# Performance work log

Measured on AMD Instinct MI355X. Metric: run time of the kernel, lower is better.

Reference implementation:

```python
import jax, jax.numpy as jnp
import numpy as np

N_NODES = 10000
N_EDGES = 160000
MUL = 128          # channel multiplicity
N_SPECIES = 10
SH_OFF = [0, 1, 4, 9, 16]   # spherical-harmonic offsets for l=0..3 (2l+1 each)
RADIAL_IN = 8
SIN_DIM = 32
MAX_DENSITY = 100.0


def setup_inputs() -> dict:
    key = jax.random.key(0)
    ks = jax.random.split(key, 16)
    inp = {
        'node_attrs': jax.random.normal(ks[0], (N_NODES, N_SPECIES), jnp.float32),
        'node_feats': jax.random.normal(ks[1], (N_NODES, MUL), jnp.float32),
        'edge_attrs': jax.random.normal(ks[2], (N_EDGES, 16), jnp.float32),
        'edge_feats': jax.random.normal(ks[3], (N_EDGES, RADIAL_IN), jnp.float32),
        'edge_index': jax.random.randint(ks[4], (2, N_EDGES), 0, N_NODES, jnp.int64),
        'W_up': jax.random.normal(ks[5], (MUL, MUL), jnp.float32),
        'Wr1': jax.random.normal(ks[6], (RADIAL_IN, 64), jnp.float32),
        'Wr2': jax.random.normal(ks[7], (64, 64), jnp.float32),
        'Wr3': jax.random.normal(ks[8], (64, 64), jnp.float32),
        'Wr4': jax.random.normal(ks[9], (64, 4 * MUL), jnp.float32),
        'Wd': jax.random.normal(ks[10], (RADIAL_IN, 1), jnp.float32),
        'Wsin': jax.random.normal(ks[11], (SIN_DIM, MUL), jnp.float32),
        'Wlin': jax.random.normal(ks[12], (4, MUL, MUL), jnp.float32),
        'Wskip': jax.random.normal(ks[13], (4, MUL, N_SPECIES, MUL), jnp.float32),
    }
    return inp


def _sinusoidal_embedding(x):
    # continuous sinusoidal embedding: dim=32, max_density=100
    half = SIN_DIM // 2
    freqs = jnp.exp(-jnp.log(MAX_DENSITY) * jnp.arange(half, dtype=x.dtype) / half)
    ang = x[:, None] * freqs[None, :]          # [N, 16]
    return jnp.concatenate([jnp.sin(ang), jnp.cos(ang)], axis=-1)  # [N, 32]


def reference(node_attrs, node_feats, edge_attrs, edge_feats, edge_index,
              W_up, Wr1, Wr2, Wr3, Wr4, Wd, Wsin, Wlin, Wskip):
    N = node_feats.shape[0]
    sender, receiver = edge_index[0], edge_index[1]

    # linear_up (e3nn o3.Linear on 128x0e, fan-in normalized)
    x = node_feats @ (W_up / np.float32(np.sqrt(MUL)))          # [N, 128]

    # radial MLP: FullyConnectedNet([8,64,64,64,512], silu), fan-in normalized
    h = edge_feats
    for W in (Wr1, Wr2, Wr3):
        h = jax.nn.silu(h @ (W / np.float32(np.sqrt(W.shape[0]))))
    tp_w = (h @ (Wr4 / np.float32(np.sqrt(64)))).reshape(-1, 4, MUL)  # [E, 4, 128]

    # equivariant TP: scalar node feats (x) gathered by sender, uvu path per SH l
    xs = x[sender]                                              # [E, 128]
    weighted = xs[:, None, :] * tp_w                            # [E, 4, 128]
    blocks = []
    for l in range(4):
        sh_l = edge_attrs[:, SH_OFF[l]:SH_OFF[l + 1]]           # [E, 2l+1]
        blk = weighted[:, l, :, None] * sh_l[:, None, :]        # [E, 128, 2l+1]
        blocks.append(blk.reshape(blk.shape[0], -1))
    mji = jnp.concatenate(blocks, axis=-1)                      # [E, 2048]

    # per-edge density gate
    density = jnp.tanh((edge_feats @ Wd) ** 2)                  # [E, 1]

    # scatter-sum messages and density to receivers
    message = jax.ops.segment_sum(mji, receiver, num_segments=N)        # [N, 2048]
    rho = jax.ops.segment_sum(density, receiver, num_segments=N)       # [N, 1]
    message = message / (rho + 1.0)

    # density embedding injected into the l=0 block
    demb = _sinusoidal_embedding(rho[:, 0]) @ Wsin              # [N, 128]
    message = message.at[:, :MUL].add(demb)

    # per-l linear (irreps_mid -> irreps_out), skip_tp with node_attrs, reshape
    out_blocks = []
    for l in range(4):
        d = 2 * l + 1
        blk = message[:, MUL * SH_OFF[l]:MUL * SH_OFF[l + 1]].reshape(N, MUL, d)
        blk = jnp.einsum('nuk,uv->nvk', blk, Wlin[l]) / np.float32(np.sqrt(MUL))
        blk = jnp.einsum('nvk,na,vaw->nwk', blk, node_attrs, Wskip[l]) \
              / np.float32(np.sqrt(MUL * N_SPECIES))
        out_blocks.append(blk)
    return jnp.concatenate(out_blocks, axis=-1)                 # [N, 128, 16]
```

## Files before the change

### kernel.cpp

```cpp
#include <hip/hip_runtime.h>
#include <hip/hip_bf16.h>

#define N_NODES 10000
#define N_EDGES 160000

typedef _Float16 h8 __attribute__((ext_vector_type(8)));
typedef _Float16 h4 __attribute__((ext_vector_type(4)));
typedef float f32x4 __attribute__((ext_vector_type(4)));

__device__ __forceinline__ float silu_f(float v){ return v / (1.f + expf(-v)); }

__global__ __launch_bounds__(256) void k_pre(const float* __restrict__ Wr2,
                                             const float* __restrict__ Wr3,
                                             const float* __restrict__ Wr4,
                                             const float* __restrict__ Wup,
                                             const float* __restrict__ Wlin,
                                             const float* __restrict__ Wskip,
                                             const int* __restrict__ eidx,
                                             _Float16* __restrict__ Wr2T,
                                             _Float16* __restrict__ Wr3T,
                                             _Float16* __restrict__ Wr4T,
                                             _Float16* __restrict__ WupT,
                                             _Float16* __restrict__ WC16T,
                                             int* __restrict__ cnt){
  const int b = blockIdx.x;
  __shared__ float wl[128];
  if (b < 224){
    const int idx = b*256 + threadIdx.x;
    if (idx < 4096){
      const int n = idx >> 6, k = idx & 63;
      Wr2T[idx] = (_Float16)(Wr2[k*64 + n] * 0.125f);
    } else if (idx < 8192){
      const int j = idx - 4096;
      const int n = j >> 6, k = j & 63;
      Wr3T[j] = (_Float16)(Wr3[k*64 + n] * 0.125f);
    } else if (idx < 40960){
      const int j = idx - 8192;
      const int n = j >> 6, k = j & 63;
      Wr4T[j] = (_Float16)(Wr4[k*512 + n] * 0.125f);
    } else if (idx < 57344){
      const int j = idx - 40960;
      const int u = j >> 7, k = j & 127;
      WupT[j] = (_Float16)(Wup[k*128 + u] * 0.08838834764831843f);
    }
  } else if (b < 736){
    const int lu = b - 224;
    const int l  = lu >> 7, u = lu & 127;
    if (threadIdx.x < 128) wl[threadIdx.x] = Wlin[lu*128 + threadIdx.x];
    __syncthreads();
    const float* Wsk = Wskip + (size_t)l * 163840;
    for (int i = threadIdx.x; i < 1280; i += 256){
      float acc = 0.f;
      #pragma unroll 16
      for (int v = 0; v < 128; ++v) acc += wl[v] * Wsk[v*1280 + i];
      const int a = i >> 7, w = i & 127;
      WC16T[((size_t)l*128 + w)*1280 + a*128 + u] =
          (_Float16)(acc * 0.0024705294220065465f);
    }
  } else {
    const int e = (b - 736)*256 + threadIdx.x;
    if (e < N_EDGES) atomicAdd(&cnt[eidx[N_EDGES + e]], 1);
  }
}

__global__ __launch_bounds__(256) void k_scan(const int* __restrict__ cnt,
                                              int* __restrict__ off,
                                              int* __restrict__ cur){
  __shared__ int sums[256];
  const int t = threadIdx.x;
  const int base = t * 40;
  int s = 0;
  for (int i = 0; i < 40; ++i){
    const int idx = base + i;
    if (idx < N_NODES) s += cnt[idx];
  }
  sums[t] = s;
  __syncthreads();
  for (int st = 1; st < 256; st <<= 1){
    const int v = (t >= st) ? sums[t - st] : 0;
    __syncthreads();
    sums[t] += v;
    __syncthreads();
  }
  int pre = (t > 0) ? sums[t - 1] : 0;
  for (int i = 0; i < 40; ++i){
    const int idx = base + i;
    if (idx < N_NODES){
      off[idx] = pre; cur[idx] = pre;
      pre += cnt[idx];
    }
  }
  if (t == 255) off[N_NODES] = sums[255];
}

__global__ __launch_bounds__(256) void k_mid(const int* __restrict__ eidx,
                                             const float* __restrict__ ef,
                                             const float* __restrict__ ea,
                                             int* __restrict__ cur,
                                             int* __restrict__ esnd,
                                             float* __restrict__ efp,
                                             float* __restrict__ eap,
                                             const float* __restrict__ nf,
                                             const _Float16* __restrict__ WupT,
                                             float* __restrict__ x){
  const int b = blockIdx.x;
  const int tid = threadIdx.x;
  alignas(16) __shared__ _Float16 s_nf[64*128];
  alignas(16) __shared__ _Float16 s_wt[128*128];

  if (b < 625){
    const int e = b * 256 + tid;
    if (e < N_EDGES){
      const int pos = atomicAdd(&cur[eidx[N_EDGES + e]], 1);
      esnd[pos] = eidx[e];
      const float4* efs = (const float4*)(ef + (size_t)e*8);
      float4* efd = (float4*)(efp + (size_t)pos*8);
      efd[0] = efs[0]; efd[1] = efs[1];
      const float4* eas = (const float4*)(ea + (size_t)e*16);
      float4* ead = (float4*)(eap + (size_t)pos*16);
      ead[0] = eas[0]; ead[1] = eas[1]; ead[2] = eas[2]; ead[3] = eas[3];
    }
    return;
  }

  const int n0 = (b - 625) * 64;
  {
    const int rl = tid >> 2, part = tid & 3;
    const int gr = n0 + rl;
    #pragma unroll
    for (int j = 0; j < 4; ++j){
      const int cu = part*4 + j;
      h8 hv = (h8){};
      if (gr < N_NODES){
        const float4 v0 = *(const float4*)(nf + (size_t)gr*128 + cu*8);
        const float4 v1 = *(const float4*)(nf + (size_t)gr*128 + cu*8 + 4);
        hv[0]=(_Float16)v0.x; hv[1]=(_Float16)v0.y; hv[2]=(_Float16)v0.z; hv[3]=(_Float16)v0.w;
        hv[4]=(_Float16)v1.x; hv[5]=(_Float16)v1.y; hv[6]=(_Float16)v1.z; hv[7]=(_Float16)v1.w;
      }
      const int cs = (cu & 8) | ((cu & 7) ^ (rl & 7));
      *(h8*)&s_nf[rl*128 + cs*8] = hv;
    }
  }
  {
    const int rl = tid >> 1, part = tid & 1;
    #pragma unroll
    for (int j = 0; j < 8; ++j){
      const int cu = part*8 + j;
      const h8 v = *(const h8*)&WupT[(size_t)rl*128 + cu*8];
      const int cs = (cu & 8) | ((cu & 7) ^ (rl & 7));
      *(h8*)&s_wt[rl*128 + cs*8] = v;
    }
  }
  __syncthreads();

  const int wid = tid >> 6, lane = tid & 63;
  const int li = lane & 15, kg = lane >> 4;

  f32x4 acc[8];
  #pragma unroll
  for (int i = 0; i < 8; ++i) acc[i] = (f32x4){0,0,0,0};

  const int row = wid*16 + li;
  #pragma unroll
  for (int s = 0; s < 4; ++s){
    const int ca = s*4 + kg;
    const int csA = (ca & 8) | ((ca & 7) ^ (row & 7));
    const h8 af = *(const h8*)&s_nf[row*128 + csA*8];
    #pragma unroll
    for (int nt = 0; nt < 8; ++nt){
      const int u = nt*16 + li;
      const int csB = (ca & 8) | ((ca & 7) ^ (u & 7));
      const h8 bf = *(const h8*)&s_wt[u*128 + csB*8];
      acc[nt] = __builtin_amdgcn_mfma_f32_16x16x32_f16(af, bf, acc[nt], 0, 0, 0);
    }
  }
  #pragma unroll
  for (int nt = 0; nt < 8; ++nt){
    #pragma unroll
    for (int r = 0; r < 4; ++r){
      const int gr = n0 + wid*16 + kg*4 + r;
      if (gr < N_NODES) x[(size_t)gr*128 + nt*16 + li] = acc[nt][r];
    }
  }
}

__global__ __launch_bounds__(256) void k_fused(const float* __restrict__ efp,
                                               const float* __restrict__ eap,
                                               const float* __restrict__ x,
                                               const float* __restrict__ Wr1,
                                               const float* __restrict__ Wd,
                                               const _Float16* __restrict__ Wr2T,
                                               const _Float16* __restrict__ Wr3T,
                                               const _Float16* __restrict__ Wr4T,
                                               const float* __restrict__ Wsin,
                                               const int* __restrict__ off,
                                               const int* __restrict__ esnd,
                                               _Float16* __restrict__ msg16){
  const int n0 = blockIdx.x * 4;
  const int tid = threadIdx.x;
  const int lane = tid & 63, wid = tid >> 6;
  const int li = lane & 15, kg = lane >> 4;
  const int u = tid & 127, h = tid >> 7;

  __shared__ float s_ef[32][8];
  __shared__ float s_w1[8][64];
  alignas(16) __shared__ _Float16 s_xs[32][132];
  alignas(16) __shared__ _Float16 s_actA[32][64];
  alignas(16) __shared__ _Float16 s_actB[32][64];
  alignas(16) __shared__ _Float16 s_w2[32][264];
  alignas(16) __shared__ float s_sh[2][32][16];
  __shared__ float s_dd[32];
  __shared__ float s_rho[4];
  __shared__ int   s_offs[5];
  __shared__ float s_emb[4][32];

  if (tid < 5) s_offs[tid] = off[n0 + tid];
  if (tid < 4) s_rho[tid] = 0.f;
  for (int j = tid; j < 512; j += 256) s_w1[j >> 6][j & 63] = Wr1[j];
  __syncthreads();

  const int beg = s_offs[0], end = s_offs[4];
  const int ngrp = (end - beg + 31) >> 5;

  const int e8 = tid >> 3, i8 = tid & 7;
  const int slotB = tid >> 4, jjB = tid & 15;

  float a0[8] = {0,0,0,0,0,0,0,0};
  float a1[8] = {0,0,0,0,0,0,0,0};
  float a2[8] = {0,0,0,0,0,0,0,0};
  float a3[8] = {0,0,0,0,0,0,0,0};

  if (ngrp > 0){
    const int p = beg + e8;
    s_ef[e8][i8] = (p < end) ? efp[(size_t)p*8 + i8] : 0.f;
    const int pB0 = beg + slotB, pB1 = beg + slotB + 16;
    s_sh[0][slotB][jjB]      = (pB0 < end) ? eap[(size_t)pB0*16 + jjB] : 0.f;
    s_sh[0][slotB + 16][jjB] = (pB1 < end) ? eap[(size_t)pB1*16 + jjB] : 0.f;
    const int snd = (p < end) ? esnd[p] : 0;
    const float4* xp = (const float4*)(x + (size_t)snd*128 + i8*16);
    #pragma unroll
    for (int j = 0; j < 4; ++j){
      const float4 v = xp[j];
      h4 hv; hv[0]=(_Float16)v.x; hv[1]=(_Float16)v.y; hv[2]=(_Float16)v.z; hv[3]=(_Float16)v.w;
      *(h4*)&s_xs[e8][i8*16 + j*4] = hv;
    }
  }
  __syncthreads();

  for (int g = 0; g < ngrp; ++g){
    const int cur = g & 1, nxt = cur ^ 1;
    const int pbase  = beg + g*32;
    const int pbase2 = pbase + 32;
    const bool more = (g + 1 < ngrp);

    float ef_r = 0.f, sh_r0 = 0.f, sh_r1 = 0.f;
    int snd_r = 0;
    const int pA = pbase2 + e8;
    const bool vA = more && (pA < end);
    if (vA){ ef_r = efp[(size_t)pA*8 + i8]; snd_r = esnd[pA]; }
    const int pB0 = pbase2 + slotB, pB1 = pbase2 + slotB + 16;
    if (more && pB0 < end) sh_r0 = eap[(size_t)pB0*16 + jjB];
    if (more && pB1 < end) sh_r1 = eap[(size_t)pB1*16 + jjB];

    if (tid < 32){
      float s = 0.f;
      #pragma unroll
      for (int i = 0; i < 8; ++i) s += s_ef[tid][i] * Wd[i];
      s_dd[tid] = tanhf(s*s);
    }

    {
      const int e = tid >> 3, ng = tid & 7;
      float hv[8] = {0,0,0,0,0,0,0,0};
      #pragma unroll
      for (int k = 0; k < 8; ++k){
        const float ev = s_ef[e][k] * 0.3535533905932738f;
        #pragma unroll
        for (int j = 0; j < 8; ++j) hv[j] += ev * s_w1[k][ng*8 + j];
      }
      h8 o;
      #pragma unroll
      for (int j = 0; j < 8; ++j) o[j] = (_Float16)silu_f(hv[j]);
      *(h8*)&s_actA[e][(ng ^ (e & 7))*8] = o;
    }
    __syncthreads();

    if (more) s_ef[e8][i8] = ef_r;

    {
      h8 af[2];
      #pragma unroll
      for (int s = 0; s < 2; ++s)
        af[s] = *(const h8*)&Wr2T[(size_t)(wid*16 + li)*64 + s*32 + kg*8];
      #pragma unroll
      for (int nt = 0; nt < 2; ++nt){
        const int e = nt*16 + li;
        f32x4 acc = (f32x4){0,0,0,0};
        #pragma unroll
        for (int s = 0; s < 2; ++s){
          const h8 bf = *(const h8*)&s_actA[e][((s*4 + kg) ^ (e & 7))*8];
          acc = __builtin_amdgcn_mfma_f32_16x16x32_f16(af[s], bf, acc, 0, 0, 0);
        }
        #pragma unroll
        for (int r = 0; r < 4; ++r){
          const int n = wid*16 + kg*4 + r;
          s_actB[e][((n >> 3) ^ (e & 7))*8 + (n & 7)] = (_Float16)silu_f(acc[r]);
        }
      }
    }
    __syncthreads();

    float4 xs_r0 = {0,0,0,0}, xs_r1 = {0,0,0,0}, xs_r2 = {0,0,0,0}, xs_r3 = {0,0,0,0};
    if (vA){
      const float4* xp = (const float4*)(x + (size_t)snd_r*128 + i8*16);
      xs_r0 = xp[0]; xs_r1 = xp[1]; xs_r2 = xp[2]; xs_r3 = xp[3];
    }

    {
      h8 af[2];
      #pragma unroll
      for (int s = 0; s < 2; ++s)
        af[s] = *(const h8*)&Wr3T[(size_t)(wid*16 + li)*64 + s*32 + kg*8];
      #pragma unroll
      for (int nt = 0; nt < 2; ++nt){
        const int e = nt*16 + li;
        f32x4 acc = (f32x4){0,0,0,0};
        #pragma unroll
        for (int s = 0; s < 2; ++s){
          const h8 bf = *(const h8*)&s_actB[e][((s*4 + kg) ^ (e & 7))*8];
          acc = __builtin_amdgcn_mfma_f32_16x16x32_f16(af[s], bf, acc, 0, 0, 0);
        }
        #pragma unroll
        for (int r = 0; r < 4; ++r){
          const int n = wid*16 + kg*4 + r;
          s_actA[e][((n >> 3) ^ (e & 7))*8 + (n & 7)] = (_Float16)silu_f(acc[r]);
        }
      }
    }
    __syncthreads();

    int lo0 = s_offs[0] - pbase; lo0 = lo0 < 0 ? 0 : lo0;
    int hi0 = s_offs[1] - pbase; hi0 = hi0 > 32 ? 32 : (hi0 < 0 ? 0 : hi0);
    int lo1 = s_offs[1] - pbase; lo1 = lo1 < 0 ? 0 : lo1;
    int hi1 = s_offs[2] - pbase; hi1 = hi1 > 32 ? 32 : (hi1 < 0 ? 0 : hi1);
    int lo2 = s_offs[2] - pbase; lo2 = lo2 < 0 ? 0 : lo2;
    int hi2 = s_offs[3] - pbase; hi2 = hi2 > 32 ? 32 : (hi2 < 0 ? 0 : hi2);
    int lo3 = s_offs[3] - pbase; lo3 = lo3 < 0 ? 0 : lo3;
    int hi3 = s_offs[4] - pbase; hi3 = hi3 > 32 ? 32 : (hi3 < 0 ? 0 : hi3);

    h8 bf[2][2];
    #pragma unroll
    for (int nt = 0; nt < 2; ++nt){
      const int e = nt*16 + li;
      #pragma unroll
      for (int s = 0; s < 2; ++s)
        bf[nt][s] = *(const h8*)&s_actA[e][((s*4 + kg) ^ (e & 7))*8];
    }

#define ACCA(A, LO, HI)                                              \
    for (int s = (LO); s < (HI); ++s){                               \
      const float wa  = (float)s_w2[s][u];                           \
      const float wb  = (float)s_w2[s][128 + u];                     \
      const float4 sa = *(const float4*)&s_sh[cur][s][0];            \
      A[0] += wa*sa.x;                                               \
      A[1] += wb*sa.y;  A[2] += wb*sa.z;  A[3] += wb*sa.w;           \
    }
#define ACCB0(A, LO, HI)                                             \
    for (int s = (LO); s < (HI); ++s){                               \
      const float wcv = (float)s_w2[s][u];                           \
      const float4 sb = *(const float4*)&s_sh[cur][s][4];            \
      A[4] += wcv*sb.x; A[5] += wcv*sb.y;                            \
      A[6] += wcv*sb.z; A[7] += wcv*sb.w;                            \
    }
#define ACCB1(A, LO, HI)                                             \
    for (int s = (LO); s < (HI); ++s){                               \
      const float wcv = (float)s_w2[s][u];                           \
      const float wd  = (float)s_w2[s][128 + u];                     \
      const float4 sa = *(const float4*)&s_sh[cur][s][8];            \
      const float4 sb = *(const float4*)&s_sh[cur][s][12];           \
      A[0] += wcv*sa.x;                                              \
      A[1] += wd*sa.y;  A[2] += wd*sa.z;  A[3] += wd*sa.w;           \
      A[4] += wd*sb.x;  A[5] += wd*sb.y;                             \
      A[6] += wd*sb.z;  A[7] += wd*sb.w;                             \
    }

    #pragma unroll
    for (int pass = 0; pass < 2; ++pass){
      #pragma unroll
      for (int mt = 0; mt < 4; ++mt){
        const int cc0 = wid*64 + mt*16;
        const int nb  = pass*256 + cc0;
        h8 af[2];
        #pragma unroll
        for (int s = 0; s < 2; ++s)
          af[s] = *(const h8*)&Wr4T[(size_t)(nb + li)*64 + s*32 + kg*8];
        f32x4 acc[2];
        #pragma unroll
        for (int nt = 0; nt < 2; ++nt){
          acc[nt] = (f32x4){0,0,0,0};
          #pragma unroll
          for (int s = 0; s < 2; ++s)
            acc[nt] = __builtin_amdgcn_mfma_f32_16x16x32_f16(af[s], bf[nt][s], acc[nt], 0, 0, 0);
        }
        const int cc = cc0 + kg*4;
        const int u0 = cc & 127;
        #pragma unroll
        for (int nt = 0; nt < 2; ++nt){
          const int e = nt*16 + li;
          const h4 xv = *(const h4*)&s_xs[e][u0];
          h4 ov;
          #pragma unroll
          for (int r = 0; r < 4; ++r) ov[r] = (_Float16)acc[nt][r] * xv[r];
          *(h4*)&s_w2[e][cc] = ov;
        }
      }
      __syncthreads();

      if (pass == 0){
        if (h == 0){
          ACCA(a0, lo0, hi0) ACCA(a1, lo1, hi1)
          ACCA(a2, lo2, hi2) ACCA(a3, lo3, hi3)
        }
      } else {
        if (h == 0){
          ACCB0(a0, lo0, hi0) ACCB0(a1, lo1, hi1)
          ACCB0(a2, lo2, hi2) ACCB0(a3, lo3, hi3)
        } else {
          ACCB1(a0, lo0, hi0) ACCB1(a1, lo1, hi1)
          ACCB1(a2, lo2, hi2) ACCB1(a3, lo3, hi3)
        }
        if (tid < 4){
          int lo = s_offs[tid]     - pbase; lo = lo < 0 ? 0 : lo;
          int hi = s_offs[tid + 1] - pbase; hi = hi > 32 ? 32 : (hi < 0 ? 0 : hi);
          float r = 0.f;
          for (int s = lo; s < hi; ++s) r += s_dd[s];
          s_rho[tid] += r;
        }
        if (more){
          s_sh[nxt][slotB][jjB]      = sh_r0;
          s_sh[nxt][slotB + 16][jjB] = sh_r1;
          const float4 xr[4] = {xs_r0, xs_r1, xs_r2, xs_r3};
          #pragma unroll
          for (int j = 0; j < 4; ++j){
            h4 hv; hv[0]=(_Float16)xr[j].x; hv[1]=(_Float16)xr[j].y;
            hv[2]=(_Float16)xr[j].z; hv[3]=(_Float16)xr[j].w;
            *(h4*)&s_xs[e8][i8*16 + j*4] = hv;
          }
        }
      }
      __syncthreads();
    }
  }

  if (tid < 64){
    const int ni = tid >> 4, f = tid & 15;
    const float fr  = expf(-0.28782313662425572f * (float)f);
    const float ang = s_rho[ni] * fr;
    s_emb[ni][f]      = sinf(ang);
    s_emb[ni][f + 16] = cosf(ang);
  }
  __syncthreads();

  float db0 = 0.f, db1 = 0.f, db2 = 0.f, db3 = 0.f;
  if (h == 0){
    #pragma unroll 8
    for (int j = 0; j < 32; ++j){
      const float wsv = Wsin[j*128 + u];
      db0 += s_emb[0][j]*wsv; db1 += s_emb[1][j]*wsv;
      db2 += s_emb[2][j]*wsv; db3 += s_emb[3][j]*wsv;
    }
  }
  const float t0 = 1.f/(s_rho[0]+1.f), t1 = 1.f/(s_rho[1]+1.f);
  const float t2 = 1.f/(s_rho[2]+1.f), t3 = 1.f/(s_rho[3]+1.f);
  #pragma unroll
  for (int j = 0; j < 8; ++j){
    float v0 = a0[j]*t0, v1 = a1[j]*t1, v2 = a2[j]*t2, v3 = a3[j]*t3;
    if (h == 0 && j == 0){ v0 += db0; v1 += db1; v2 += db2; v3 += db3; }
    const size_t base = (size_t)(h*8 + j)*128 + u;
    msg16[(size_t)(n0+0)*2048 + base] = (_Float16)v0;
    msg16[(size_t)(n0+1)*2048 + base] = (_Float16)v1;
    msg16[(size_t)(n0+2)*2048 + base] = (_Float16)v2;
    msg16[(size_t)(n0+3)*2048 + base] = (_Float16)v3;
  }
}

template<int L, int D>
__device__ __forceinline__ void final_body(const int bb,
                                           const _Float16* __restrict__ msg16,
                                           const float* __restrict__ attrs,
                                           const _Float16* __restrict__ WC16T,
                                           _Float16* __restrict__ outD,
                                           _Float16* __restrict__ sA,
                                           _Float16* __restrict__ sB,
                                           _Float16* __restrict__ sAttr){
  constexpr int OFF  = (L==0 ? 0 : L==1 ? 1 : L==2 ? 4 : 9);
  constexpr int ROWS = N_NODES * D;
  const int r0  = bb * 128;
  const int tid = threadIdx.x;

  {
    const int rl = tid >> 2, quarter = tid & 3;
    const int gr = r0 + rl;
    h8 vals[4];
    if (gr < ROWS){
      const int n = gr / D, k = gr - n*D;
      const _Float16* src = msg16 + (size_t)n*2048 + (size_t)(OFF+k)*128 + quarter*32;
      #pragma unroll
      for (int j = 0; j < 4; ++j) vals[j] = *(const h8*)(src + j*8);
    } else {
      #pragma unroll
      for (int j = 0; j < 4; ++j) vals[j] = (h8){};
    }
    #pragma unroll
    for (int j = 0; j < 4; ++j){
      const int cu = quarter*4 + j;
      const int cs = (cu & 8) | ((cu & 7) ^ (rl & 7));
      *(h8*)&sA[rl*128 + cs*8] = vals[j];
    }
  }
  for (int i = tid; i < 1280; i += 512){
    const int rl = i / 10, aa = i - rl*10;
    const int gr = r0 + rl;
    sAttr[i] = (gr < ROWS) ? (_Float16)attrs[(gr / D)*10 + aa] : (_Float16)0.f;
  }
  {
    const int w = tid >> 2, part = tid & 3;
    const _Float16* src = WC16T + ((size_t)L*128 + w)*1280 + part*16;
    #pragma unroll
    for (int j = 0; j < 2; ++j){
      const h8 v = *(const h8*)(src + j*8);
      const int cc = part*2 + j;
      *(h8*)&sB[w*64 + (cc ^ (w & 7))*8] = v;
    }
  }
  __syncthreads();

  const int wid = tid >> 6, lane = tid & 63;
  const int wm = wid >> 2, wn = wid & 3;
  const int li = lane & 15, kg = lane >> 4;

  f32x4 acc[4][2];
  #pragma unroll
  for (int m = 0; m < 4; ++m)
    #pragma unroll
    for (int nn = 0; nn < 2; ++nn) acc[m][nn] = (f32x4){0,0,0,0};

  for (int step = 0; step < 20; ++step){
    _Float16* sbc = (step & 1) ? (sB + 8192) : sB;
    _Float16* sbn = (step & 1) ? sB : (sB + 8192);
    const bool more = (step + 1 < 20);
    h8 pre[2];
    if (more){
      const int a2 = (step+1) >> 1, u02 = ((step+1) & 1) << 6;
      const _Float16* src = WC16T + ((size_t)L*128 + (tid>>2))*1280 + a2*128 + u02 + (tid&3)*16;
      #pragma unroll
      for (int j = 0; j < 2; ++j) pre[j] = *(const h8*)(src + j*8);
    }

    const int a  = step >> 1;
    const int uh = (step & 1) << 3;

    h8 afr[4][2], bfr[2][2];
    #pragma unroll
    for (int m = 0; m < 4; ++m){
      const int row = wm*64 + m*16 + li;
      const _Float16 av = sAttr[row*10 + a];
      h8 avx;
      #pragma unroll
      for (int j = 0; j < 8; ++j) avx[j] = av;
      #pragma unroll
      for (int s = 0; s < 2; ++s){
        const int ca = uh + s*4 + kg;
        const int cs = (ca & 8) | ((ca & 7) ^ (row & 7));
        const h8 mA = *(const h8*)&sA[row*128 + cs*8];
        afr[m][s] = mA * avx;
      }
    }
    #pragma unroll
    for (int nn = 0; nn < 2; ++nn){
      const int w = wn*32 + nn*16 + li;
      #pragma unroll
      for (int s = 0; s < 2; ++s){
        const int cb = s*4 + kg;
        bfr[nn][s] = *(const h8*)&sbc[w*64 + ((cb ^ (w & 7)))*8];
      }
    }
    #pragma unroll
    for (int s = 0; s < 2; ++s)
      #pragma unroll
      for (int m = 0; m < 4; ++m)
        #pragma unroll
        for (int nn = 0; nn < 2; ++nn)
          acc[m][nn] = __builtin_amdgcn_mfma_f32_16x16x32_f16(afr[m][s], bfr[nn][s], acc[m][nn], 0, 0, 0);

    if (more){
      const int w = tid >> 2, part = tid & 3;
      #pragma unroll
      for (int j = 0; j < 2; ++j){
        const int cc = part*2 + j;
        *(h8*)&sbn[w*64 + (cc ^ (w & 7))*8] = pre[j];
      }
    }
    __syncthreads();
  }

  #pragma unroll
  for (int m = 0; m < 4; ++m){
    const int rbase = r0 + wm*64 + m*16 + kg*4;
    #pragma unroll
    for (int rr = 0; rr < 4; ++rr){
      const int gr = rbase + rr;
      if (gr < ROWS){
        _Float16* op = outD + (size_t)gr*128;
        #pragma unroll
        for (int nn = 0; nn < 2; ++nn)
          op[wn*32 + nn*16 + li] = (_Float16)acc[m][nn][rr];
      }
    }
  }
}

__global__ __launch_bounds__(512) void k_final_all(const _Float16* __restrict__ msg16,
                                                   const float* __restrict__ attrs,
                                                   const _Float16* __restrict__ WC16T,
                                                   _Float16* __restrict__ outD){
  alignas(16) __shared__ _Float16 sA[128*128];
  alignas(16) __shared__ _Float16 sB[2*64*128];
  __shared__ _Float16 sAttr[128*10];
  const int b = blockIdx.x;
  if (b < 79)       final_body<0,1>(b,       msg16, attrs, WC16T, outD,            sA, sB, sAttr);
  else if (b < 314) final_body<1,3>(b - 79,  msg16, attrs, WC16T, outD + 1280000,  sA, sB, sAttr);
  else if (b < 705) final_body<2,5>(b - 314, msg16, attrs, WC16T, outD + 5120000,  sA, sB, sAttr);
  else              final_body<3,7>(b - 705, msg16, attrs, WC16T, outD + 11520000, sA, sB, sAttr);
}

__global__ __launch_bounds__(256) void k_merge(const _Float16* __restrict__ outD,
                                               float* __restrict__ out){
  const int n0 = blockIdx.x * 4;
  const int tid = threadIdx.x;
  __shared__ float lds[4*16*132];

#define MERGE_LOAD(SRC, CHUNKS, ROWS_PER_N, SKOFF)                       \
  { const _Float16* src = (SRC);                                         \
    for (int j = tid; j < (CHUNKS); j += 256){                           \
      const int row = j >> 4, c8 = j & 15;                               \
      const int nloc = row / (ROWS_PER_N), k = row - nloc*(ROWS_PER_N);  \
      const h8 v = *(const h8*)(src + (size_t)row*128 + c8*8);           \
      float* dst = &lds[(nloc*16 + (SKOFF) + k)*132 + c8*8];             \
      dst[0]=(float)v[0]; dst[1]=(float)v[1]; dst[2]=(float)v[2];        \
      dst[3]=(float)v[3]; dst[4]=(float)v[4]; dst[5]=(float)v[5];        \
      dst[6]=(float)v[6]; dst[7]=(float)v[7];                            \
    } }

  MERGE_LOAD(outD + (size_t)n0*128,                 64,  1, 0)
  MERGE_LOAD(outD + 1280000 + (size_t)n0*3*128,    192,  3, 1)
  MERGE_LOAD(outD + 5120000 + (size_t)n0*5*128,    320,  5, 4)
  MERGE_LOAD(outD + 11520000 + (size_t)n0*7*128,   448,  7, 9)
  __syncthreads();

  for (int j = tid; j < 2048; j += 256){
    const int nloc = j >> 9, qv = j & 511;
    const int w = qv >> 2, s0 = (qv & 3) << 2;
    float4 v;
    v.x = lds[(nloc*16 + s0 + 0)*132 + w];
    v.y = lds[(nloc*16 + s0 + 1)*132 + w];
    v.z = lds[(nloc*16 + s0 + 2)*132 + w];
    v.w = lds[(nloc*16 + s0 + 3)*132 + w];
    *(float4*)&out[(size_t)(n0 + nloc)*2048 + qv*4] = v;
  }
}

extern "C" void kernel_launch(void* const* d_in, const int* in_sizes, int n_in,
                              void* d_out, int out_size, void* d_ws, size_t ws_size,
                              hipStream_t stream){
  const float* node_attrs = (const float*)d_in[0];
  const float* node_feats = (const float*)d_in[1];
  const float* edge_attrs = (const float*)d_in[2];
  const float* edge_feats = (const float*)d_in[3];
  const int*   edge_index = (const int*)d_in[4];
  const float* W_up  = (const float*)d_in[5];
  const float* Wr1   = (const float*)d_in[6];
  const float* Wr2   = (const float*)d_in[7];
  const float* Wr3   = (const float*)d_in[8];
  const float* Wr4   = (const float*)d_in[9];
  const float* Wd    = (const float*)d_in[10];
  const float* Wsin  = (const float*)d_in[11];
  const float* Wlin  = (const float*)d_in[12];
  const float* Wskip = (const float*)d_in[13];
  float* out = (float*)d_out;

  _Float16* outD  = (_Float16*)d_ws;
  _Float16* msg16 = outD + 20480000;
  float* x        = (float*)(msg16 + 20480000);
  _Float16* WC16T = (_Float16*)(x + 1280000);
  int* cnt   = (int*)(WC16T + 655360);
  int* off   = cnt + 10000;
  int* cur   = off + 10016;
  int* esnd  = cur + 10000;
  float* efp = (float*)(esnd + 160000);
  float* eap = efp + 1280000;
  _Float16* Wr2T = (_Float16*)(eap + 2560000);
  _Float16* Wr3T = Wr2T + 4096;
  _Float16* Wr4T = Wr3T + 4096;
  _Float16* WupT = Wr4T + 32768;

  hipMemsetAsync(cnt, 0, (size_t)10000 * sizeof(int), stream);

  k_pre<<<1361, 256, 0, stream>>>(Wr2, Wr3, Wr4, W_up, Wlin, Wskip, edge_index,
                                  Wr2T, Wr3T, Wr4T, WupT, WC16T, cnt);
  k_scan<<<1, 256, 0, stream>>>(cnt, off, cur);
  k_mid<<<782, 256, 0, stream>>>(edge_index, edge_feats, edge_attrs,
                                 cur, esnd, efp, eap,
                                 node_feats, WupT, x);

  k_fused<<<N_NODES/4, 256, 0, stream>>>(efp, eap, x,
                                         Wr1, Wd, Wr2T, Wr3T, Wr4T, Wsin,
                                         off, esnd, msg16);

  k_final_all<<<1252, 512, 0, stream>>>(msg16, node_attrs, WC16T, outD);

  k_merge<<<2500, 256, 0, stream>>>(outD, out);
}
```

Before: 315.0 us.

## Replace scalar per-edge scatter accumulation with MFMA over masked spherical-harmonic tiles

The tensor-product/scatter step that summed edge messages into the four receiver nodes used scalar FMAs over LDS. It becomes MFMA matmuls: the spherical harmonics are stored transposed in fp16, masked per receiver segment, and multiplied with a transposed weight-times-feature buffer covering all 512 channels in one pass. The scheme computes all 16 SH components per l-block and discards the unneeded ones at write-out. In exchange it uses 128 accumulator registers per thread and does redundant MFMA work, which may lower occupancy. The edge features and sender features are double-buffered, which also cuts the number of barriers per group.

```diff
diff --git a/kernel.cpp b/kernel.cpp
--- a/kernel.cpp
+++ b/kernel.cpp
@@ -202,17 +202,18 @@
   const int li = lane & 15, kg = lane >> 4;
   const int u = tid & 127, h = tid >> 7;
 
-  __shared__ float s_ef[32][8];
+  __shared__ float s_ef[2][32][8];
   __shared__ float s_w1[8][64];
-  alignas(16) __shared__ _Float16 s_xs[32][132];
+  alignas(16) __shared__ _Float16 s_xs[2][32][132];
   alignas(16) __shared__ _Float16 s_actA[32][64];
   alignas(16) __shared__ _Float16 s_actB[32][64];
-  alignas(16) __shared__ _Float16 s_w2[32][264];
-  alignas(16) __shared__ float s_sh[2][32][16];
+  alignas(16) __shared__ _Float16 s_w2T[512][40];
+  alignas(16) __shared__ _Float16 s_shT[2][16][40];
   __shared__ float s_dd[32];
   __shared__ float s_rho[4];
   __shared__ int   s_offs[5];
   __shared__ float s_emb[4][32];
+  __shared__ float s_demb[4][128];
 
   if (tid < 5) s_offs[tid] = off[n0 + tid];
   if (tid < 4) s_rho[tid] = 0.f;
@@ -225,24 +226,26 @@
   const int e8 = tid >> 3, i8 = tid & 7;
   const int slotB = tid >> 4, jjB = tid & 15;
 
-  float a0[8] = {0,0,0,0,0,0,0,0};
-  float a1[8] = {0,0,0,0,0,0,0,0};
-  float a2[8] = {0,0,0,0,0,0,0,0};
-  float a3[8] = {0,0,0,0,0,0,0,0};
+  f32x4 acc0[8], acc1[8], acc2[8], acc3[8];
+  #pragma unroll
+  for (int t = 0; t < 8; ++t){
+    acc0[t] = (f32x4){0,0,0,0}; acc1[t] = (f32x4){0,0,0,0};
+    acc2[t] = (f32x4){0,0,0,0}; acc3[t] = (f32x4){0,0,0,0};
+  }
 
   if (ngrp > 0){
     const int p = beg + e8;
-    s_ef[e8][i8] = (p < end) ? efp[(size_t)p*8 + i8] : 0.f;
+    s_ef[0][e8][i8] = (p < end) ? efp[(size_t)p*8 + i8] : 0.f;
     const int pB0 = beg + slotB, pB1 = beg + slotB + 16;
-    s_sh[0][slotB][jjB]      = (pB0 < end) ? eap[(size_t)pB0*16 + jjB] : 0.f;
-    s_sh[0][slotB + 16][jjB] = (pB1 < end) ? eap[(size_t)pB1*16 + jjB] : 0.f;
+    s_shT[0][jjB][slotB]      = (pB0 < end) ? (_Float16)eap[(size_t)pB0*16 + jjB] : (_Float16)0.f;
+    s_shT[0][jjB][slotB + 16] = (pB1 < end) ? (_Float16)eap[(size_t)pB1*16 + jjB] : (_Float16)0.f;
     const int snd = (p < end) ? esnd[p] : 0;
     const float4* xp = (const float4*)(x + (size_t)snd*128 + i8*16);
     #pragma unroll
     for (int j = 0; j < 4; ++j){
       const float4 v = xp[j];
       h4 hv; hv[0]=(_Float16)v.x; hv[1]=(_Float16)v.y; hv[2]=(_Float16)v.z; hv[3]=(_Float16)v.w;
-      *(h4*)&s_xs[e8][i8*16 + j*4] = hv;
+      *(h4*)&s_xs[0][e8][i8*16 + j*4] = hv;
     }
   }
   __syncthreads();
@@ -265,7 +268,7 @@
     if (tid < 32){
       float s = 0.f;
       #pragma unroll
-      for (int i = 0; i < 8; ++i) s += s_ef[tid][i] * Wd[i];
+      for (int i = 0; i < 8; ++i) s += s_ef[cur][tid][i] * Wd[i];
       s_dd[tid] = tanhf(s*s);
     }
 
@@ -274,7 +277,7 @@
       float hv[8] = {0,0,0,0,0,0,0,0};
       #pragma unroll
       for (int k = 0; k < 8; ++k){
-        const float ev = s_ef[e][k] * 0.3535533905932738f;
+        const float ev = s_ef[cur][e][k] * 0.3535533905932738f;
         #pragma unroll
         for (int j = 0; j < 8; ++j) hv[j] += ev * s_w1[k][ng*8 + j];
       }
@@ -284,8 +287,6 @@
       *(h8*)&s_actA[e][(ng ^ (e & 7))*8] = o;
     }
     __syncthreads();
-
-    if (more) s_ef[e8][i8] = ef_r;
 
     {
       h8 af[2];
@@ -334,6 +335,47 @@
         for (int r = 0; r < 4; ++r){
           const int n = wid*16 + kg*4 + r;
           s_actA[e][((n >> 3) ^ (e & 7))*8 + (n & 7)] = (_Float16)silu_f(acc[r]);
+        }
+      }
+    }
+    __syncthreads();
+
+    {
+      h8 bf[2][2];
+      #pragma unroll
+      for (int nt = 0; nt < 2; ++nt){
+        const int e = nt*16 + li;
+        #pragma unroll
+        for (int s = 0; s < 2; ++s)
+          bf[nt][s] = *(const h8*)&s_actA[e][((s*4 + kg) ^ (e & 7))*8];
+      }
+      #pragma unroll
+      for (int p = 0; p < 2; ++p){
+        #pragma unroll
+        for (int mt = 0; mt < 4; ++mt){
+          const int nbase = wid*128 + p*64 + mt*16;
+          h8 af[2];
+          #pragma unroll
+          for (int s = 0; s < 2; ++s)
+            af[s] = *(const h8*)&Wr4T[(size_t)(nbase + li)*64 + s*32 + kg*8];
+          f32x4 acc[2];
+          #pragma unroll
+          for (int nt = 0; nt < 2; ++nt){
+            acc[nt] = (f32x4){0,0,0,0};
+            #pragma unroll
+            for (int s = 0; s < 2; ++s)
+              acc[nt] = __builtin_amdgcn_mfma_f32_16x16x32_f16(af[s], bf[nt][s], acc[nt], 0, 0, 0);
+          }
+          const int c0 = nbase + kg*4;
+          const int u0 = c0 & 127;
+          #pragma unroll
+          for (int nt = 0; nt < 2; ++nt){
+            const int e = nt*16 + li;
+            const h4 xv = *(const h4*)&s_xs[cur][e][u0];
+            #pragma unroll
+            for (int r = 0; r < 4; ++r)
+              s_w2T[c0 + r][e] = (_Float16)acc[nt][r] * xv[r];
+          }
         }
       }
     }
@@ -348,108 +390,48 @@
     int lo3 = s_offs[3] - pbase; lo3 = lo3 < 0 ? 0 : lo3;
     int hi3 = s_offs[4] - pbase; hi3 = hi3 > 32 ? 32 : (hi3 < 0 ? 0 : hi3);
 
-    h8 bf[2][2];
-    #pragma unroll
-    for (int nt = 0; nt < 2; ++nt){
-      const int e = nt*16 + li;
-      #pragma unroll
-      for (int s = 0; s < 2; ++s)
-        bf[nt][s] = *(const h8*)&s_actA[e][((s*4 + kg) ^ (e & 7))*8];
-    }
-
-#define ACCA(A, LO, HI)                                              \
-    for (int s = (LO); s < (HI); ++s){                               \
-      const float wa  = (float)s_w2[s][u];                           \
-      const float wb  = (float)s_w2[s][128 + u];                     \
-      const float4 sa = *(const float4*)&s_sh[cur][s][0];            \
-      A[0] += wa*sa.x;                                               \
-      A[1] += wb*sa.y;  A[2] += wb*sa.z;  A[3] += wb*sa.w;           \
-    }
-#define ACCB0(A, LO, HI)                                             \
-    for (int s = (LO); s < (HI); ++s){                               \
-      const float wcv = (float)s_w2[s][u];                           \
-      const float4 sb = *(const float4*)&s_sh[cur][s][4];            \
-      A[4] += wcv*sb.x; A[5] += wcv*sb.y;                            \
-      A[6] += wcv*sb.z; A[7] += wcv*sb.w;                            \
-    }
-#define ACCB1(A, LO, HI)                                             \
-    for (int s = (LO); s < (HI); ++s){                               \
-      const float wcv = (float)s_w2[s][u];                           \
-      const float wd  = (float)s_w2[s][128 + u];                     \
-      const float4 sa = *(const float4*)&s_sh[cur][s][8];            \
-      const float4 sb = *(const float4*)&s_sh[cur][s][12];           \
-      A[0] += wcv*sa.x;                                              \
-      A[1] += wd*sa.y;  A[2] += wd*sa.z;  A[3] += wd*sa.w;           \
-      A[4] += wd*sb.x;  A[5] += wd*sb.y;                             \
-      A[6] += wd*sb.z;  A[7] += wd*sb.w;                             \
-    }
-
-    #pragma unroll
-    for (int pass = 0; pass < 2; ++pass){
-      #pragma unroll
-      for (int mt = 0; mt < 4; ++mt){
-        const int cc0 = wid*64 + mt*16;
-        const int nb  = pass*256 + cc0;
-        h8 af[2];
-        #pragma unroll
-        for (int s = 0; s < 2; ++s)
-          af[s] = *(const h8*)&Wr4T[(size_t)(nb + li)*64 + s*32 + kg*8];
-        f32x4 acc[2];
-        #pragma unroll
-        for (int nt = 0; nt < 2; ++nt){
-          acc[nt] = (f32x4){0,0,0,0};
-          #pragma unroll
-          for (int s = 0; s < 2; ++s)
-            acc[nt] = __builtin_amdgcn_mfma_f32_16x16x32_f16(af[s], bf[nt][s], acc[nt], 0, 0, 0);
-        }
-        const int cc = cc0 + kg*4;
-        const int u0 = cc & 127;
-        #pragma unroll
-        for (int nt = 0; nt < 2; ++nt){
-          const int e = nt*16 + li;
-          const h4 xv = *(const h4*)&s_xs[e][u0];
-          h4 ov;
-          #pragma unroll
-          for (int r = 0; r < 4; ++r) ov[r] = (_Float16)acc[nt][r] * xv[r];
-          *(h4*)&s_w2[e][cc] = ov;
-        }
-      }
-      __syncthreads();
-
-      if (pass == 0){
-        if (h == 0){
-          ACCA(a0, lo0, hi0) ACCA(a1, lo1, hi1)
-          ACCA(a2, lo2, hi2) ACCA(a3, lo3, hi3)
-        }
-      } else {
-        if (h == 0){
-          ACCB0(a0, lo0, hi0) ACCB0(a1, lo1, hi1)
-          ACCB0(a2, lo2, hi2) ACCB0(a3, lo3, hi3)
-        } else {
-          ACCB1(a0, lo0, hi0) ACCB1(a1, lo1, hi1)
-          ACCB1(a2, lo2, hi2) ACCB1(a3, lo3, hi3)
-        }
-        if (tid < 4){
-          int lo = s_offs[tid]     - pbase; lo = lo < 0 ? 0 : lo;
-          int hi = s_offs[tid + 1] - pbase; hi = hi > 32 ? 32 : (hi < 0 ? 0 : hi);
-          float r = 0.f;
-          for (int s = lo; s < hi; ++s) r += s_dd[s];
-          s_rho[tid] += r;
-        }
-        if (more){
-          s_sh[nxt][slotB][jjB]      = sh_r0;
-          s_sh[nxt][slotB + 16][jjB] = sh_r1;
-          const float4 xr[4] = {xs_r0, xs_r1, xs_r2, xs_r3};
-          #pragma unroll
-          for (int j = 0; j < 4; ++j){
-            h4 hv; hv[0]=(_Float16)xr[j].x; hv[1]=(_Float16)xr[j].y;
-            hv[2]=(_Float16)xr[j].z; hv[3]=(_Float16)xr[j].w;
-            *(h4*)&s_xs[e8][i8*16 + j*4] = hv;
-          }
-        }
-      }
-      __syncthreads();
-    }
+    {
+      const h8 afF = *(const h8*)&s_shT[cur][li][kg*8];
+      h8 af0 = afF, af1 = afF, af2 = afF, af3 = afF;
+      #pragma unroll
+      for (int j = 0; j < 8; ++j){
+        const int slot = kg*8 + j;
+        if (slot < lo0 || slot >= hi0) af0[j] = (_Float16)0.f;
+        if (slot < lo1 || slot >= hi1) af1[j] = (_Float16)0.f;
+        if (slot < lo2 || slot >= hi2) af2[j] = (_Float16)0.f;
+        if (slot < lo3 || slot >= hi3) af3[j] = (_Float16)0.f;
+      }
+      #pragma unroll
+      for (int t = 0; t < 8; ++t){
+        const h8 bf = *(const h8*)&s_w2T[wid*128 + t*16 + li][kg*8];
+        acc0[t] = __builtin_amdgcn_mfma_f32_16x16x32_f16(af0, bf, acc0[t], 0, 0, 0);
+        acc1[t] = __builtin_amdgcn_mfma_f32_16x16x32_f16(af1, bf, acc1[t], 0, 0, 0);
+        acc2[t] = __builtin_amdgcn_mfma_f32_16x16x32_f16(af2, bf, acc2[t], 0, 0, 0);
+        acc3[t] = __builtin_amdgcn_mfma_f32_16x16x32_f16(af3, bf, acc3[t], 0, 0, 0);
+      }
+    }
+
+    if (tid < 4){
+      int lo = s_offs[tid]     - pbase; lo = lo < 0 ? 0 : lo;
+      int hi = s_offs[tid + 1] - pbase; hi = hi > 32 ? 32 : (hi < 0 ? 0 : hi);
+      float r = 0.f;
+      for (int s = lo; s < hi; ++s) r += s_dd[s];
+      s_rho[tid] += r;
+    }
+
+    if (more){
+      s_ef[nxt][e8][i8] = ef_r;
+      s_shT[nxt][jjB][slotB]      = (_Float16)sh_r0;
+      s_shT[nxt][jjB][slotB + 16] = (_Float16)sh_r1;
+      const float4 xr[4] = {xs_r0, xs_r1, xs_r2, xs_r3};
+      #pragma unroll
+      for (int j = 0; j < 4; ++j){
+        h4 hv; hv[0]=(_Float16)xr[j].x; hv[1]=(_Float16)xr[j].y;
+        hv[2]=(_Float16)xr[j].z; hv[3]=(_Float16)xr[j].w;
+        *(h4*)&s_xs[nxt][e8][i8*16 + j*4] = hv;
+      }
+    }
+    __syncthreads();
   }
 
   if (tid < 64){
@@ -460,27 +442,44 @@
     s_emb[ni][f + 16] = cosf(ang);
   }
   __syncthreads();
-
-  float db0 = 0.f, db1 = 0.f, db2 = 0.f, db3 = 0.f;
   if (h == 0){
+    float db0 = 0.f, db1 = 0.f, db2 = 0.f, db3 = 0.f;
     #pragma unroll 8
     for (int j = 0; j < 32; ++j){
       const float wsv = Wsin[j*128 + u];
       db0 += s_emb[0][j]*wsv; db1 += s_emb[1][j]*wsv;
       db2 += s_emb[2][j]*wsv; db3 += s_emb[3][j]*wsv;
     }
-  }
+    s_demb[0][u] = db0; s_demb[1][u] = db1;
+    s_demb[2][u] = db2; s_demb[3][u] = db3;
+  }
+  __syncthreads();
+
   const float t0 = 1.f/(s_rho[0]+1.f), t1 = 1.f/(s_rho[1]+1.f);
   const float t2 = 1.f/(s_rho[2]+1.f), t3 = 1.f/(s_rho[3]+1.f);
+  const int OFFl = (wid==0) ? 0 : (wid==1) ? 1 : (wid==2) ? 4 : 9;
+  const int Dl   = 2*wid + 1;
+
   #pragma unroll
-  for (int j = 0; j < 8; ++j){
-    float v0 = a0[j]*t0, v1 = a1[j]*t1, v2 = a2[j]*t2, v3 = a3[j]*t3;
-    if (h == 0 && j == 0){ v0 += db0; v1 += db1; v2 += db2; v3 += db3; }
-    const size_t base = (size_t)(h*8 + j)*128 + u;
-    msg16[(size_t)(n0+0)*2048 + base] = (_Float16)v0;
-    msg16[(size_t)(n0+1)*2048 + base] = (_Float16)v1;
-    msg16[(size_t)(n0+2)*2048 + base] = (_Float16)v2;
-    msg16[(size_t)(n0+3)*2048 + base] = (_Float16)v3;
+  for (int t = 0; t < 8; ++t){
+    const int uu = t*16 + li;
+    #pragma unroll
+    for (int r = 0; r < 4; ++r){
+      const int sk = kg*4 + r;
+      if (sk >= OFFl && sk < OFFl + Dl){
+        const size_t base = (size_t)sk*128 + uu;
+        float v0 = acc0[t][r]*t0, v1 = acc1[t][r]*t1;
+        float v2 = acc2[t][r]*t2, v3 = acc3[t][r]*t3;
+        if (wid == 0 && sk == 0){
+          v0 += s_demb[0][uu]; v1 += s_demb[1][uu];
+          v2 += s_demb[2][uu]; v3 += s_demb[3][uu];
+        }
+        msg16[(size_t)(n0+0)*2048 + base] = (_Float16)v0;
+        msg16[(size_t)(n0+1)*2048 + base] = (_Float16)v1;
+        msg16[(size_t)(n0+2)*2048 + base] = (_Float16)v2;
+        msg16[(size_t)(n0+3)*2048 + base] = (_Float16)v3;
+      }
+    }
   }
 }
 
```

Result: slower. 408.8 us (+29.8%).
